# Optimization experiments

Hardware: AMD Instinct MI355X
Metric: run time of the kernel (lower is better)

## Reference

```python
import jax, jax.numpy as jnp
import numpy as np

N_U, N_R, D, H, E = 100000, 50000, 128, 64, 1000000


def setup_inputs() -> dict:
    key = jax.random.key(0)
    ks = jax.random.split(key, 12)
    s = 1.0 / np.sqrt(D)
    return {
        "x_user": jax.random.normal(ks[0], (N_U, D), jnp.float32),
        "x_res": jax.random.normal(ks[1], (N_R, D), jnp.float32),
        "edge_ua_src": jax.random.randint(ks[2], (E,), 0, N_U),
        "edge_ua_dst": jax.random.randint(ks[3], (E,), 0, N_R),
        "edge_ru_src": jax.random.randint(ks[4], (E,), 0, N_R),
        "edge_ru_dst": jax.random.randint(ks[5], (E,), 0, N_U),
        "W_l_ua": jax.random.normal(ks[6], (D, H), jnp.float32) * s,
        "b_ua": jax.random.normal(ks[7], (H,), jnp.float32) * s,
        "W_r_ua": jax.random.normal(ks[8], (D, H), jnp.float32) * s,
        "W_l_ru": jax.random.normal(ks[9], (D, H), jnp.float32) * s,
        "b_ru": jax.random.normal(ks[10], (H,), jnp.float32) * s,
        "W_r_ru": jax.random.normal(ks[11], (D, H), jnp.float32) * s,
    }


def _sage(x_src, x_dst, src, dst, n_dst, W_l, b_l, W_r):
    # gather neighbor feats, scatter-mean onto dst nodes (0 for isolated nodes)
    agg = jax.ops.segment_sum(x_src[src], dst, num_segments=n_dst)  # [n_dst, D]
    cnt = jax.ops.segment_sum(jnp.ones((src.shape[0], 1), x_src.dtype), dst,
                              num_segments=n_dst)
    mean = agg / jnp.maximum(cnt, 1.0)
    # SAGEConv: lin_l(mean neighbor) + bias + lin_r(self), no bias on lin_r
    return mean @ W_l + b_l + x_dst @ W_r


def reference(x_user, x_res, edge_ua_src, edge_ua_dst, edge_ru_src, edge_ru_dst,
              W_l_ua, b_ua, W_r_ua, W_l_ru, b_ru, W_r_ru):
    out_res = jax.nn.relu(_sage(x_user, x_res, edge_ua_src, edge_ua_dst, N_R,
                                W_l_ua, b_ua, W_r_ua))
    out_user = jax.nn.relu(_sage(x_res, x_user, edge_ru_src, edge_ru_dst, N_U,
                                 W_l_ru, b_ru, W_r_ru))
    return out_user, out_res
```

## Files before the change

kernel.cpp:

```cpp
#include <hip/hip_runtime.h>

#define N_U 100000
#define N_R 50000
#define DIM 128
#define HID 64
#define NE  1000000

#define BROWS 128
#define NB_R ((N_R + BROWS - 1) / BROWS)
#define NB_U ((N_U + BROWS - 1) / BROWS)
#define NBKT (NB_R + NB_U)
#define N_TOT (N_R + N_U)
#define MAXB 800
#define CHUNK 4096
#define BINGRID ((NE + CHUNK - 1) / CHUNK)
#define NBIN (2 * BINGRID)
#define CAPR 3072
#define CAPU 1536
#define SCAP CAPR
#define GU2 ((N_U + 127) / 128)
#define GR2 ((N_R + 127) / 128)
#define NPROJ (GU2 + GR2)
#define NPREP (NBIN + NPROJ)
#define TRIPLE (3 * NBIN)
#define LDSU 9856

typedef unsigned int uint;
typedef __attribute__((ext_vector_type(8))) short      bf16x8;
typedef __attribute__((ext_vector_type(4))) float      f32x4;
typedef __attribute__((ext_vector_type(2))) float      f32x2;
typedef __attribute__((ext_vector_type(8))) unsigned short u16x8;

__device__ inline uint bf16_rne(float f) {
    uint u = __float_as_uint(f);
    u += 0x7FFFu + ((u >> 16) & 1u);
    return u >> 16;
}
__device__ inline float bf_lo(uint v) { return __uint_as_float(v << 16); }
__device__ inline float bf_hi(uint v) { return __uint_as_float(v & 0xFFFF0000u); }

__device__ inline uint cvt_pk_bf16(float lo, float hi) {
    uint r;
    asm("v_cvt_pk_bf16_f32 %0, %1, %2" : "=v"(r) : "v"(lo), "v"(hi));
    return r;
}

__device__ inline void pk_acc(f32x2& acc, uint v) {
    f32x2 val;
    val[0] = __uint_as_float(v << 16);
    val[1] = __uint_as_float(v & 0xFFFF0000u);
    asm("v_pk_add_f32 %0, %1, %2" : "+v"(acc) : "v"(val));
}

__device__ inline int bucket_base(int b) {
    return (b < NB_R) ? b * CAPR : NB_R * CAPR + (b - NB_R) * CAPU;
}

__global__ __launch_bounds__(256) void wcvt_kernel(
    const float* __restrict__ Wlua, const float* __restrict__ Wlru,
    const float* __restrict__ Wrua, const float* __restrict__ Wrru,
    unsigned short* __restrict__ Wbf, int* __restrict__ cur)
{
    if (blockIdx.x < 4) {
        const float* Ws[4] = {Wlua, Wlru, Wrua, Wrru};
        const float* W = Ws[blockIdx.x];
        unsigned short* dst = Wbf + blockIdx.x * 8192;
        for (int i = threadIdx.x; i < 1024; i += 256) {
            int k8 = i >> 6, col = i & 63;
            u16x8 p;
#pragma unroll
            for (int j = 0; j < 8; ++j)
                p[j] = (unsigned short)bf16_rne(W[(k8 * 8 + j) * HID + col]);
            *(u16x8*)&dst[i * 8] = p;
        }
    } else {
        int i = (blockIdx.x - 4) * 256 + threadIdx.x;
        if (i < NBKT) cur[i] = 0;
    }
}

__global__ __launch_bounds__(512, 4) void prep_kernel(
    const int* __restrict__ srcA, const int* __restrict__ dstA,
    const int* __restrict__ srcB, const int* __restrict__ dstB,
    int* __restrict__ cur, int* __restrict__ rec,
    const float* __restrict__ xu, const float* __restrict__ xr,
    const unsigned short* __restrict__ Wbf,
    const float* __restrict__ b_ua, const float* __restrict__ b_ru,
    uint* __restrict__ h_user, uint* __restrict__ h_res,
    uint* __restrict__ sbuf)
{
    __shared__ __align__(16) uint lds[LDSU];

    const int bid = blockIdx.x;
    const int t = threadIdx.x;
    int binid = -1, projid = -1;
    if (bid < TRIPLE) {
        if (bid % 3 == 0) binid = bid / 3;
        else projid = (bid / 3) * 2 + (bid % 3 - 1);
    } else {
        projid = 2 * NBIN + (bid - TRIPLE);
    }

    if (binid >= 0) {
        int* cntL = (int*)lds;
        int* offL = cntL + MAXB;
        int* curL = offL + MAXB;
        int* gbase = curL + MAXB;
        int* srec = gbase + MAXB;
        unsigned short* sbkt = (unsigned short*)(lds + 7296);
        int* tmp = (int*)(lds + 9344);

        const int seg = (binid >= BINGRID) ? 1 : 0;
        const int blk = binid - seg * BINGRID;
        const int* __restrict__ src = seg ? srcB : srcA;
        const int* __restrict__ dst = seg ? dstB : dstA;
        const int nbkt   = seg ? NB_U : NB_R;
        const int bktOff = seg ? NB_R : 0;

        const int e0 = blk * CHUNK;
        const int nhere = min(CHUNK, NE - e0);

        for (int i = t; i < nbkt; i += 512) cntL[i] = 0;
        __syncthreads();

        int myB[8], myR[8];
#pragma unroll
        for (int l = 0; l < 8; ++l) {
            int i = e0 + l * 512 + t;
            if (i < NE) {
                int d = dst[i];
                myB[l] = d >> 7;
                myR[l] = ((d & 127) << 17) | src[i];
                atomicAdd(&cntL[myB[l]], 1);
            } else myB[l] = -1;
        }
        __syncthreads();

        int vals[4], s = 0;
#pragma unroll
        for (int l = 0; l < 4; ++l) {
            int idx = t * 4 + l;
            vals[l] = (idx < nbkt) ? cntL[idx] : 0;
            s += vals[l];
        }
        tmp[t] = s;
        __syncthreads();
        for (int o = 1; o < 512; o <<= 1) {
            int v = (t >= o) ? tmp[t - o] : 0;
            __syncthreads();
            tmp[t] += v;
            __syncthreads();
        }
        int run = tmp[t] - s;
#pragma unroll
        for (int l = 0; l < 4; ++l) {
            int idx = t * 4 + l;
            if (idx < nbkt) { offL[idx] = run; curL[idx] = run; }
            run += vals[l];
        }
        __syncthreads();

        for (int i = t; i < nbkt; i += 512)
            if (cntL[i] > 0)
                gbase[i] = bucket_base(bktOff + i) + atomicAdd(&cur[bktOff + i], cntL[i]);

#pragma unroll
        for (int l = 0; l < 8; ++l) {
            if (myB[l] >= 0) {
                int slot = atomicAdd(&curL[myB[l]], 1);
                srec[slot] = myR[l];
                sbkt[slot] = (unsigned short)myB[l];
            }
        }
        __syncthreads();

        for (int sI = t; sI < nhere; sI += 512) {
            int b = sbkt[sI];
            rec[gbase[b] + (sI - offL[b])] = srec[sI];
        }
        return;
    }

    int blk, nrows;
    const float *x, *bias;
    const unsigned short *w0g, *w1g;
    uint* hb; uint* sb;
    if (projid < GU2) {
        blk = projid; x = xu; w0g = Wbf; w1g = Wbf + 3 * 8192; bias = b_ru;
        hb = h_user; sb = sbuf; nrows = N_U;
    } else {
        blk = projid - GU2; x = xr; w0g = Wbf + 1 * 8192; w1g = Wbf + 2 * 8192;
        bias = b_ua; hb = h_res; sb = sbuf + (size_t)N_U * 32; nrows = N_R;
    }

    const int rowbase = blk * 128;

    {
        const uint4* s0 = (const uint4*)w0g;
        const uint4* s1 = (const uint4*)w1g;
        uint4* d0 = (uint4*)lds;
        uint4* d1 = (uint4*)(lds + 4096);
        for (int i = t; i < 1024; i += 512) { d0[i] = s0[i]; d1[i] = s1[i]; }
    }

    const int wv = t >> 6, l = t & 63;
    const int lrow = l & 15, lk = l >> 4;
    const int myrow = rowbase + wv * 16 + lrow;
    const bool valid = myrow < nrows;
    const float4* xp = (const float4*)(x + (size_t)myrow * DIM + lk * 8);

    float4 z = make_float4(0.f, 0.f, 0.f, 0.f);
    float4 x0a = z, x0b = z, x1a = z, x1b = z, x2a = z, x2b = z, x3a = z, x3b = z;
    if (valid) {
        x0a = xp[0];  x0b = xp[1];
        x1a = xp[8];  x1b = xp[9];
        x2a = xp[16]; x2b = xp[17];
        x3a = xp[24]; x3b = xp[25];
    }
    __syncthreads();

    f32x4 acc0[4], acc1[4];
#pragma unroll
    for (int n = 0; n < 4; ++n) { acc0[n] = (f32x4)0.f; acc1[n] = (f32x4)0.f; }

#define KKSTEP(KK, XA, XB)                                                        \
    {                                                                             \
        union { uint4 u; bf16x8 v; } af;                                          \
        af.u.x = cvt_pk_bf16(XA.x, XA.y);                                         \
        af.u.y = cvt_pk_bf16(XA.z, XA.w);                                         \
        af.u.z = cvt_pk_bf16(XB.x, XB.y);                                         \
        af.u.w = cvt_pk_bf16(XB.z, XB.w);                                         \
        const int k8 = KK * 4 + lk;                                               \
        _Pragma("unroll")                                                         \
        for (int n = 0; n < 4; ++n) {                                             \
            const int col = n * 16 + lrow;                                        \
            bf16x8 b0 = *(const bf16x8*)&lds[(k8 * 64 + col) * 4];                \
            bf16x8 b1 = *(const bf16x8*)&lds[4096 + (k8 * 64 + col) * 4];         \
            acc0[n] = __builtin_amdgcn_mfma_f32_16x16x32_bf16(af.v, b0, acc0[n], 0, 0, 0); \
            acc1[n] = __builtin_amdgcn_mfma_f32_16x16x32_bf16(af.v, b1, acc1[n], 0, 0, 0); \
        }                                                                         \
    }
    KKSTEP(0, x0a, x0b)
    KKSTEP(1, x1a, x1b)
    KKSTEP(2, x2a, x2b)
    KKSTEP(3, x3a, x3b)
#undef KKSTEP

#pragma unroll
    for (int n = 0; n < 4; ++n) {
        float bv = bias[n * 16 + lrow];
#pragma unroll
        for (int r = 0; r < 4; ++r) acc1[n][r] += bv;
    }

    __syncthreads();
    uint* hA = lds;
    uint* hS = lds + 4608;
#pragma unroll
    for (int n = 0; n < 4; ++n) {
#pragma unroll
        for (int r = 0; r < 4; ++r) {
            int row = wv * 16 + lk * 4 + r;
            float hm = acc0[n][r], ho = __shfl_xor(hm, 1);
            float sm = acc1[n][r], so = __shfl_xor(sm, 1);
            if (!(lrow & 1)) {
                int c2 = n * 8 + (lrow >> 1);
                hA[row * 36 + c2] = cvt_pk_bf16(hm, ho);
                hS[row * 36 + c2] = cvt_pk_bf16(sm, so);
            }
        }
    }
    __syncthreads();
    for (int i = t; i < 128 * 8; i += 512) {
        int r = i >> 3, q = i & 7;
        if (rowbase + r < nrows) {
            *(uint4*)(hb + (size_t)(rowbase + r) * 32 + q * 4) =
                *(const uint4*)&hA[r * 36 + q * 4];
            *(uint4*)(sb + (size_t)(rowbase + r) * 32 + q * 4) =
                *(const uint4*)&hS[r * 36 + q * 4];
        }
    }
}

__global__ __launch_bounds__(512) void csr_gather_kernel(
    const int* __restrict__ rec, const int* __restrict__ cur,
    const uint* __restrict__ hu, const uint* __restrict__ hr,
    const uint* __restrict__ sbuf, float* __restrict__ out)
{
    __shared__ int srecA[SCAP];
    __shared__ int srecB[SCAP];
    __shared__ int cntL[BROWS], offL[BROWS], curL[BROWS];

    const int t = threadIdx.x;
    const int bkt = blockIdx.x;
    int lrow0, nrows, cap;
    size_t rowOff;
    const uint* __restrict__ h;
    if (bkt < NB_R) {
        lrow0 = bkt * BROWS; nrows = N_R; cap = CAPR; h = hu; rowOff = N_U;
    } else {
        lrow0 = (bkt - NB_R) * BROWS; nrows = N_U; cap = CAPU; h = hr; rowOff = 0;
    }

    const int rbase = bucket_base(bkt);
    const int rcnt  = min(cur[bkt], cap);

    if (t < BROWS) cntL[t] = 0;
    __syncthreads();
    for (int i = t; i < rcnt; i += 512) {
        int r = rec[rbase + i];
        srecA[i] = r;
        atomicAdd(&cntL[r >> 17], 1);
    }
    __syncthreads();
    if (t < BROWS) offL[t] = cntL[t];
    __syncthreads();
    for (int o = 1; o < BROWS; o <<= 1) {
        int v = (t < BROWS && t >= o) ? offL[t - o] : 0;
        __syncthreads();
        if (t < BROWS) offL[t] += v;
        __syncthreads();
    }
    if (t < BROWS) curL[t] = offL[t] - cntL[t];
    __syncthreads();
    for (int i = t; i < rcnt; i += 512) {
        int r = srecA[i];
        int slot = atomicAdd(&curL[r >> 17], 1);
        srecB[slot] = r;
    }
    __syncthreads();

    const int team = t >> 5, l32 = t & 31;
    const int q  = l32 >> 3;
    const int cl = l32 & 7;

    for (int r = team; r < BROWS; r += 16) {
        const int lr = lrow0 + r;
        if (lr >= nrows) continue;
        const int d = cntL[r];
        const int base = offL[r] - cntL[r];
        const uint* srow = sbuf + (rowOff + lr) * 32;
        float* orow = out + (rowOff + lr) * 64;

        float s0 = 0.f, s1 = 0.f, s2 = 0.f, s3 = 0.f;
        float s4 = 0.f, s5 = 0.f, s6 = 0.f, s7 = 0.f;
        if (l32 < 8) {
            uint4 sv = *(const uint4*)(srow + cl * 4);
            s0 = bf_lo(sv.x); s1 = bf_hi(sv.x); s2 = bf_lo(sv.y); s3 = bf_hi(sv.y);
            s4 = bf_lo(sv.z); s5 = bf_hi(sv.z); s6 = bf_lo(sv.w); s7 = bf_hi(sv.w);
        }

        f32x2 A0 = {0.f, 0.f}, A1 = {0.f, 0.f}, A2 = {0.f, 0.f}, A3 = {0.f, 0.f};
#define ACC(v) { pk_acc(A0, v.x); pk_acc(A1, v.y); pk_acc(A2, v.z); pk_acc(A3, v.w); }
        const uint4 z4 = make_uint4(0u, 0u, 0u, 0u);
        for (int j = 0; j < d; j += 16) {
            uint4 v0 = z4, v1 = z4, v2 = z4, v3 = z4;
            if (j + q < d)
                v0 = *(const uint4*)(h + (size_t)(srecB[base + j + q] & 0x1FFFF) * 32 + cl * 4);
            if (j + 4 + q < d)
                v1 = *(const uint4*)(h + (size_t)(srecB[base + j + 4 + q] & 0x1FFFF) * 32 + cl * 4);
            if (j + 8 + q < d)
                v2 = *(const uint4*)(h + (size_t)(srecB[base + j + 8 + q] & 0x1FFFF) * 32 + cl * 4);
            if (j + 12 + q < d)
                v3 = *(const uint4*)(h + (size_t)(srecB[base + j + 12 + q] & 0x1FFFF) * 32 + cl * 4);
            ACC(v0) ACC(v1) ACC(v2) ACC(v3)
        }
#undef ACC

#pragma unroll
        for (int off = 8; off <= 16; off <<= 1) {
            A0[0] += __shfl_xor(A0[0], off); A0[1] += __shfl_xor(A0[1], off);
            A1[0] += __shfl_xor(A1[0], off); A1[1] += __shfl_xor(A1[1], off);
            A2[0] += __shfl_xor(A2[0], off); A2[1] += __shfl_xor(A2[1], off);
            A3[0] += __shfl_xor(A3[0], off); A3[1] += __shfl_xor(A3[1], off);
        }

        if (l32 < 8) {
            float invd = 1.0f / fmaxf((float)d, 1.0f);
            float4 rA, rB;
            rA.x = fmaxf(A0[0] * invd + s0, 0.f);
            rA.y = fmaxf(A0[1] * invd + s1, 0.f);
            rA.z = fmaxf(A1[0] * invd + s2, 0.f);
            rA.w = fmaxf(A1[1] * invd + s3, 0.f);
            rB.x = fmaxf(A2[0] * invd + s4, 0.f);
            rB.y = fmaxf(A2[1] * invd + s5, 0.f);
            rB.z = fmaxf(A3[0] * invd + s6, 0.f);
            rB.w = fmaxf(A3[1] * invd + s7, 0.f);
            *(float4*)(orow + cl * 8) = rA;
            *(float4*)(orow + cl * 8 + 4) = rB;
        }
    }
}

extern "C" void kernel_launch(void* const* d_in, const int* in_sizes, int n_in,
                              void* d_out, int out_size, void* d_ws, size_t ws_size,
                              hipStream_t stream)
{
    const float* x_user = (const float*)d_in[0];
    const float* x_res  = (const float*)d_in[1];
    const int* ua_src   = (const int*)d_in[2];
    const int* ua_dst   = (const int*)d_in[3];
    const int* ru_src   = (const int*)d_in[4];
    const int* ru_dst   = (const int*)d_in[5];
    const float* W_l_ua = (const float*)d_in[6];
    const float* b_ua   = (const float*)d_in[7];
    const float* W_r_ua = (const float*)d_in[8];
    const float* W_l_ru = (const float*)d_in[9];
    const float* b_ru   = (const float*)d_in[10];
    const float* W_r_ru = (const float*)d_in[11];

    uint* h_user = (uint*)d_ws;
    uint* h_res  = h_user + (size_t)N_U * 32;
    uint* sbuf   = h_res + (size_t)N_R * 32;
    unsigned short* Wbf = (unsigned short*)(sbuf + (size_t)N_TOT * 32);
    int*  cur    = (int*)(Wbf + 4 * 8192);
    int*  rec    = cur + NBKT;

    wcvt_kernel<<<4 + (NBKT + 255) / 256, 256, 0, stream>>>(
        W_l_ua, W_l_ru, W_r_ua, W_r_ru, Wbf, cur);

    prep_kernel<<<NPREP, 512, 0, stream>>>(
        ua_src, ua_dst, ru_src, ru_dst, cur, rec,
        x_user, x_res, Wbf, b_ua, b_ru, h_user, h_res, sbuf);

    csr_gather_kernel<<<NBKT, 512, 0, stream>>>(
        rec, cur, h_user, h_res, sbuf, (float*)d_out);
}
```

Before: 91.12 us.

## Halve resource-node buckets, drop staging LDS array, gather two rows per team

```diff
diff --git a/kernel.cpp b/kernel.cpp
--- a/kernel.cpp
+++ b/kernel.cpp
@@ -6,18 +6,17 @@
 #define HID 64
 #define NE  1000000
 
-#define BROWS 128
-#define NB_R ((N_R + BROWS - 1) / BROWS)
-#define NB_U ((N_U + BROWS - 1) / BROWS)
+#define NB_R ((N_R + 63) / 64)
+#define NB_U ((N_U + 127) / 128)
 #define NBKT (NB_R + NB_U)
 #define N_TOT (N_R + N_U)
 #define MAXB 800
 #define CHUNK 4096
 #define BINGRID ((NE + CHUNK - 1) / CHUNK)
 #define NBIN (2 * BINGRID)
-#define CAPR 3072
-#define CAPU 1536
-#define SCAP CAPR
+#define CAP_R 1600
+#define CAP_U 1536
+#define SCAP 1600
 #define GU2 ((N_U + 127) / 128)
 #define GR2 ((N_R + 127) / 128)
 #define NPROJ (GU2 + GR2)
@@ -53,7 +52,7 @@
 }
 
 __device__ inline int bucket_base(int b) {
-    return (b < NB_R) ? b * CAPR : NB_R * CAPR + (b - NB_R) * CAPU;
+    return (b < NB_R) ? b * CAP_R : NB_R * CAP_R + (b - NB_R) * CAP_U;
 }
 
 __global__ __launch_bounds__(256) void wcvt_kernel(
@@ -129,8 +128,9 @@
             int i = e0 + l * 512 + t;
             if (i < NE) {
                 int d = dst[i];
-                myB[l] = d >> 7;
-                myR[l] = ((d & 127) << 17) | src[i];
+                myB[l] = seg ? (d >> 7) : (d >> 6);
+                myR[l] = seg ? (((d & 127) << 17) | src[i])
+                             : (((d & 63) << 17) | src[i]);
                 atomicAdd(&cntL[myB[l]], 1);
             } else myB[l] = -1;
         }
@@ -287,44 +287,40 @@
     const uint* __restrict__ hu, const uint* __restrict__ hr,
     const uint* __restrict__ sbuf, float* __restrict__ out)
 {
-    __shared__ int srecA[SCAP];
     __shared__ int srecB[SCAP];
-    __shared__ int cntL[BROWS], offL[BROWS], curL[BROWS];
+    __shared__ int cntL[128], offL[128], curL[128];
 
     const int t = threadIdx.x;
     const int bkt = blockIdx.x;
-    int lrow0, nrows, cap;
+    int lrow0, nrows, brows, cap;
     size_t rowOff;
     const uint* __restrict__ h;
     if (bkt < NB_R) {
-        lrow0 = bkt * BROWS; nrows = N_R; cap = CAPR; h = hu; rowOff = N_U;
+        lrow0 = bkt * 64; brows = 64; nrows = N_R; cap = CAP_R; h = hu; rowOff = N_U;
     } else {
-        lrow0 = (bkt - NB_R) * BROWS; nrows = N_U; cap = CAPU; h = hr; rowOff = 0;
+        lrow0 = (bkt - NB_R) * 128; brows = 128; nrows = N_U; cap = CAP_U; h = hr; rowOff = 0;
     }
 
     const int rbase = bucket_base(bkt);
     const int rcnt  = min(cur[bkt], cap);
 
-    if (t < BROWS) cntL[t] = 0;
+    if (t < 128) cntL[t] = 0;
+    __syncthreads();
+    for (int i = t; i < rcnt; i += 512)
+        atomicAdd(&cntL[rec[rbase + i] >> 17], 1);
+    __syncthreads();
+    if (t < 128) offL[t] = cntL[t];
+    __syncthreads();
+    for (int o = 1; o < 128; o <<= 1) {
+        int v = (t < 128 && t >= o) ? offL[t - o] : 0;
+        __syncthreads();
+        if (t < 128) offL[t] += v;
+        __syncthreads();
+    }
+    if (t < 128) curL[t] = offL[t] - cntL[t];
     __syncthreads();
     for (int i = t; i < rcnt; i += 512) {
         int r = rec[rbase + i];
-        srecA[i] = r;
-        atomicAdd(&cntL[r >> 17], 1);
-    }
-    __syncthreads();
-    if (t < BROWS) offL[t] = cntL[t];
-    __syncthreads();
-    for (int o = 1; o < BROWS; o <<= 1) {
-        int v = (t < BROWS && t >= o) ? offL[t - o] : 0;
-        __syncthreads();
-        if (t < BROWS) offL[t] += v;
-        __syncthreads();
-    }
-    if (t < BROWS) curL[t] = offL[t] - cntL[t];
-    __syncthreads();
-    for (int i = t; i < rcnt; i += 512) {
-        int r = srecA[i];
         int slot = atomicAdd(&curL[r >> 17], 1);
         srecB[slot] = r;
     }
@@ -333,39 +329,53 @@
     const int team = t >> 5, l32 = t & 31;
     const int q  = l32 >> 3;
     const int cl = l32 & 7;
-
-    for (int r = team; r < BROWS; r += 16) {
-        const int lr = lrow0 + r;
-        if (lr >= nrows) continue;
-        const int d = cntL[r];
-        const int base = offL[r] - cntL[r];
-        const uint* srow = sbuf + (rowOff + lr) * 32;
-        float* orow = out + (rowOff + lr) * 64;
-
-        float s0 = 0.f, s1 = 0.f, s2 = 0.f, s3 = 0.f;
-        float s4 = 0.f, s5 = 0.f, s6 = 0.f, s7 = 0.f;
+    const int half = brows >> 1;
+
+    for (int r0 = team; r0 < half; r0 += 16) {
+        const int rA_ = r0, rB_ = r0 + half;
+        const int lrA = lrow0 + rA_, lrB = lrow0 + rB_;
+        const bool vA = lrA < nrows, vB = lrB < nrows;
+        const int dA = vA ? cntL[rA_] : 0, dB = vB ? cntL[rB_] : 0;
+        const int baseA = offL[rA_] - cntL[rA_], baseB = offL[rB_] - cntL[rB_];
+
+        float sA[8] = {0}, sB[8] = {0};
         if (l32 < 8) {
-            uint4 sv = *(const uint4*)(srow + cl * 4);
-            s0 = bf_lo(sv.x); s1 = bf_hi(sv.x); s2 = bf_lo(sv.y); s3 = bf_hi(sv.y);
-            s4 = bf_lo(sv.z); s5 = bf_hi(sv.z); s6 = bf_lo(sv.w); s7 = bf_hi(sv.w);
-        }
-
-        f32x2 A0 = {0.f, 0.f}, A1 = {0.f, 0.f}, A2 = {0.f, 0.f}, A3 = {0.f, 0.f};
-#define ACC(v) { pk_acc(A0, v.x); pk_acc(A1, v.y); pk_acc(A2, v.z); pk_acc(A3, v.w); }
+            if (vA) {
+                uint4 sv = *(const uint4*)(sbuf + (rowOff + lrA) * 32 + cl * 4);
+                sA[0] = bf_lo(sv.x); sA[1] = bf_hi(sv.x); sA[2] = bf_lo(sv.y); sA[3] = bf_hi(sv.y);
+                sA[4] = bf_lo(sv.z); sA[5] = bf_hi(sv.z); sA[6] = bf_lo(sv.w); sA[7] = bf_hi(sv.w);
+            }
+            if (vB) {
+                uint4 sv = *(const uint4*)(sbuf + (rowOff + lrB) * 32 + cl * 4);
+                sB[0] = bf_lo(sv.x); sB[1] = bf_hi(sv.x); sB[2] = bf_lo(sv.y); sB[3] = bf_hi(sv.y);
+                sB[4] = bf_lo(sv.z); sB[5] = bf_hi(sv.z); sB[6] = bf_lo(sv.w); sB[7] = bf_hi(sv.w);
+            }
+        }
+
+        f32x2 A0 = {0,0}, A1 = {0,0}, A2 = {0,0}, A3 = {0,0};
+        f32x2 B0 = {0,0}, B1 = {0,0}, B2 = {0,0}, B3 = {0,0};
         const uint4 z4 = make_uint4(0u, 0u, 0u, 0u);
-        for (int j = 0; j < d; j += 16) {
-            uint4 v0 = z4, v1 = z4, v2 = z4, v3 = z4;
-            if (j + q < d)
-                v0 = *(const uint4*)(h + (size_t)(srecB[base + j + q] & 0x1FFFF) * 32 + cl * 4);
-            if (j + 4 + q < d)
-                v1 = *(const uint4*)(h + (size_t)(srecB[base + j + 4 + q] & 0x1FFFF) * 32 + cl * 4);
-            if (j + 8 + q < d)
-                v2 = *(const uint4*)(h + (size_t)(srecB[base + j + 8 + q] & 0x1FFFF) * 32 + cl * 4);
-            if (j + 12 + q < d)
-                v3 = *(const uint4*)(h + (size_t)(srecB[base + j + 12 + q] & 0x1FFFF) * 32 + cl * 4);
-            ACC(v0) ACC(v1) ACC(v2) ACC(v3)
-        }
-#undef ACC
+        const int dmax = max(dA, dB);
+        for (int j = 0; j < dmax; j += 16) {
+            uint4 a0 = z4, a1 = z4, a2 = z4, a3 = z4;
+            uint4 b0 = z4, b1 = z4, b2 = z4, b3 = z4;
+            if (j + q < dA)      a0 = *(const uint4*)(h + (size_t)(srecB[baseA + j + q] & 0x1FFFF) * 32 + cl * 4);
+            if (j + 4 + q < dA)  a1 = *(const uint4*)(h + (size_t)(srecB[baseA + j + 4 + q] & 0x1FFFF) * 32 + cl * 4);
+            if (j + 8 + q < dA)  a2 = *(const uint4*)(h + (size_t)(srecB[baseA + j + 8 + q] & 0x1FFFF) * 32 + cl * 4);
+            if (j + 12 + q < dA) a3 = *(const uint4*)(h + (size_t)(srecB[baseA + j + 12 + q] & 0x1FFFF) * 32 + cl * 4);
+            if (j + q < dB)      b0 = *(const uint4*)(h + (size_t)(srecB[baseB + j + q] & 0x1FFFF) * 32 + cl * 4);
+            if (j + 4 + q < dB)  b1 = *(const uint4*)(h + (size_t)(srecB[baseB + j + 4 + q] & 0x1FFFF) * 32 + cl * 4);
+            if (j + 8 + q < dB)  b2 = *(const uint4*)(h + (size_t)(srecB[baseB + j + 8 + q] & 0x1FFFF) * 32 + cl * 4);
+            if (j + 12 + q < dB) b3 = *(const uint4*)(h + (size_t)(srecB[baseB + j + 12 + q] & 0x1FFFF) * 32 + cl * 4);
+            pk_acc(A0, a0.x); pk_acc(A1, a0.y); pk_acc(A2, a0.z); pk_acc(A3, a0.w);
+            pk_acc(A0, a1.x); pk_acc(A1, a1.y); pk_acc(A2, a1.z); pk_acc(A3, a1.w);
+            pk_acc(A0, a2.x); pk_acc(A1, a2.y); pk_acc(A2, a2.z); pk_acc(A3, a2.w);
+            pk_acc(A0, a3.x); pk_acc(A1, a3.y); pk_acc(A2, a3.z); pk_acc(A3, a3.w);
+            pk_acc(B0, b0.x); pk_acc(B1, b0.y); pk_acc(B2, b0.z); pk_acc(B3, b0.w);
+            pk_acc(B0, b1.x); pk_acc(B1, b1.y); pk_acc(B2, b1.z); pk_acc(B3, b1.w);
+            pk_acc(B0, b2.x); pk_acc(B1, b2.y); pk_acc(B2, b2.z); pk_acc(B3, b2.w);
+            pk_acc(B0, b3.x); pk_acc(B1, b3.y); pk_acc(B2, b3.z); pk_acc(B3, b3.w);
+        }
 
 #pragma unroll
         for (int off = 8; off <= 16; off <<= 1) {
@@ -373,21 +383,43 @@
             A1[0] += __shfl_xor(A1[0], off); A1[1] += __shfl_xor(A1[1], off);
             A2[0] += __shfl_xor(A2[0], off); A2[1] += __shfl_xor(A2[1], off);
             A3[0] += __shfl_xor(A3[0], off); A3[1] += __shfl_xor(A3[1], off);
+            B0[0] += __shfl_xor(B0[0], off); B0[1] += __shfl_xor(B0[1], off);
+            B1[0] += __shfl_xor(B1[0], off); B1[1] += __shfl_xor(B1[1], off);
+            B2[0] += __shfl_xor(B2[0], off); B2[1] += __shfl_xor(B2[1], off);
+            B3[0] += __shfl_xor(B3[0], off); B3[1] += __shfl_xor(B3[1], off);
         }
 
         if (l32 < 8) {
-            float invd = 1.0f / fmaxf((float)d, 1.0f);
-            float4 rA, rB;
-            rA.x = fmaxf(A0[0] * invd + s0, 0.f);
-            rA.y = fmaxf(A0[1] * invd + s1, 0.f);
-            rA.z = fmaxf(A1[0] * invd + s2, 0.f);
-            rA.w = fmaxf(A1[1] * invd + s3, 0.f);
-            rB.x = fmaxf(A2[0] * invd + s4, 0.f);
-            rB.y = fmaxf(A2[1] * invd + s5, 0.f);
-            rB.z = fmaxf(A3[0] * invd + s6, 0.f);
-            rB.w = fmaxf(A3[1] * invd + s7, 0.f);
-            *(float4*)(orow + cl * 8) = rA;
-            *(float4*)(orow + cl * 8 + 4) = rB;
+            if (vA) {
+                float invd = 1.0f / fmaxf((float)dA, 1.0f);
+                float* orow = out + (rowOff + lrA) * 64;
+                float4 rA, rB2;
+                rA.x = fmaxf(A0[0] * invd + sA[0], 0.f);
+                rA.y = fmaxf(A0[1] * invd + sA[1], 0.f);
+                rA.z = fmaxf(A1[0] * invd + sA[2], 0.f);
+                rA.w = fmaxf(A1[1] * invd + sA[3], 0.f);
+                rB2.x = fmaxf(A2[0] * invd + sA[4], 0.f);
+                rB2.y = fmaxf(A2[1] * invd + sA[5], 0.f);
+                rB2.z = fmaxf(A3[0] * invd + sA[6], 0.f);
+                rB2.w = fmaxf(A3[1] * invd + sA[7], 0.f);
+                *(float4*)(orow + cl * 8) = rA;
+                *(float4*)(orow + cl * 8 + 4) = rB2;
+            }
+            if (vB) {
+                float invd = 1.0f / fmaxf((float)dB, 1.0f);
+                float* orow = out + (rowOff + lrB) * 64;
+                float4 rA, rB2;
+                rA.x = fmaxf(B0[0] * invd + sB[0], 0.f);
+                rA.y = fmaxf(B0[1] * invd + sB[1], 0.f);
+                rA.z = fmaxf(B1[0] * invd + sB[2], 0.f);
+                rA.w = fmaxf(B1[1] * invd + sB[3], 0.f);
+                rB2.x = fmaxf(B2[0] * invd + sB[4], 0.f);
+                rB2.y = fmaxf(B2[1] * invd + sB[5], 0.f);
+                rB2.z = fmaxf(B3[0] * invd + sB[6], 0.f);
+                rB2.w = fmaxf(B3[1] * invd + sB[7], 0.f);
+                *(float4*)(orow + cl * 8) = rA;
+                *(float4*)(orow + cl * 8 + 4) = rB2;
+            }
         }
     }
 }
```

Result: slower. 95.75 us (+5.1%).
